# Kernel tuning notes

Measured on AMD Instinct MI355X. Metric: run time of the kernel, lower is better.

The kernel has to match this reference:

```python
import jax, jax.numpy as jnp
import numpy as np
from jax.scipy.special import i0

# --- NUFFT adjoint (Kaiser-Bessel gridding) configuration ---
N = 512            # image side (image_shape)
K = 2 * N
M = 200_000        # n_measurements (visibilities)
B = 8              # batch of measurement vectors
J = 6              # gridding kernel width (plan uses (6, 6))
BETA = 2.34 * J


def setup_inputs() -> dict:
    key = jax.random.key(0)
    k1, k2, k3 = jax.random.split(key, 3)
    # uv coordinates in [-pi, pi) radians per pixel (standard NUFFT convention)
    uv = jax.random.uniform(k1, (M, 2), jnp.float32, -np.pi, np.pi)
    y_real = jax.random.normal(k2, (B, M), jnp.float32)
    y_imag = jax.random.normal(k3, (B, M), jnp.float32)
    weights = jnp.ones((M,), jnp.float32)  # measurement_weights
    return {"y_real": y_real, "y_imag": y_imag, "uv": uv, "weights": weights}


def _grid_1d(coord):
    """Per-axis gridding indices and Kaiser-Bessel weights.

    coord: (M,) frequencies in [-pi, pi). Returns idx (M, J) int32 grid
    columns (wrapped mod K) and w (M, J) float32 kernel weights.
    """
    k = coord / (2.0 * np.pi) * K            # grid units, in [-K/2, K/2)
    km = jnp.floor(k - J / 2.0)              # leftmost neighbor base
    j = jnp.arange(1, J + 1, dtype=k.dtype)
    pts = km[:, None] + j                    # (M, J) grid points covered
    d = k[:, None] - pts                     # signed distance, |d| <= J/2
    arg = jnp.maximum(1.0 - (2.0 * d / J) ** 2, 0.0)
    w = i0(BETA * jnp.sqrt(arg)) / i0(jnp.float32(BETA))
    idx = jnp.mod(pts, K).astype(jnp.int32)
    return idx, w.astype(jnp.float32)


def _deapod(n):
    """Gridding-correction (inverse FT of the KB kernel) at image pixels."""
    x = (jnp.arange(n, dtype=jnp.float32) - n / 2.0) / K
    t = BETA ** 2 - (np.pi * J * x) ** 2
    st = jnp.sqrt(jnp.abs(t))
    num = jnp.where(t > 0, jnp.sinh(st), jnp.sin(st))
    return num / jnp.maximum(st, 1e-6)


def reference(y_real, y_imag, uv, weights):
    y = (y_real + 1j * y_imag).astype(jnp.complex64) * weights  # (B, M)

    ix, wx = _grid_1d(uv[:, 0])  # (M, J)
    iy, wy = _grid_1d(uv[:, 1])  # (M, J)

    # Separable 6x6 kernel: outer products per measurement
    flat_idx = (ix[:, :, None] * K + iy[:, None, :]).reshape(-1)        # (M*J*J,)
    w2 = (wx[:, :, None] * wy[:, None, :]).reshape(M, J * J)            # (M, 36)
    vals = (y[:, :, None] * w2[None]).reshape(B, -1)                    # (B, M*36)

    # Scatter-add onto the oversampled grid (duplicate indices accumulate)
    grid = jnp.zeros((B, K * K), jnp.complex64).at[:, flat_idx].add(vals)
    grid = grid.reshape(B, K, K)

    # Unnormalized inverse FFT (adjoint of the forward FFT), shift to center
    img = jnp.fft.fftshift(jnp.fft.ifft2(grid), axes=(-2, -1)) * (K * K)

    # Crop central N x N region and de-apodize
    s = (K - N) // 2
    img_c = jnp.real(img[:, s:s + N, s:s + N])
    apod = _deapod(N)
    return img_c / (apod[:, None] * apod[None, :])
```

## Files before the change

### kernel.cpp

```cpp
#include <hip/hip_runtime.h>
#include <hip/hip_fp16.h>
#include <math.h>

#define KGRID 1024
#define NIMG  512
#define JW    6
#define BETAF 14.04f
#define NB    8
#define NBIN  16384
#define CAP   96

typedef float v2f __attribute__((ext_vector_type(2)));
typedef float v4f __attribute__((ext_vector_type(4)));

__device__ __forceinline__ float i0f_dev(float x) {
    float ax = fabsf(x);
    if (ax < 3.75f) {
        float z = ax * (1.0f / 3.75f);
        z = z * z;
        return 1.0f + z * (3.5156229f + z * (3.0899424f + z * (1.2067492f +
               z * (0.2659732f + z * (0.0360768f + z * 0.0045813f)))));
    } else {
        float z = 3.75f / ax;
        float p = 0.39894228f + z * (0.01328592f + z * (0.00225319f + z * (-0.00157565f +
                  z * (0.00916281f + z * (-0.02057706f + z * (0.02635537f +
                  z * (-0.01647633f + z * 0.00392377f)))))));
        return expf(ax) * rsqrtf(ax) * p;
    }
}

__global__ __launch_bounds__(256) void prep_kernel(
    const float* __restrict__ yr, const float* __restrict__ yi,
    const float* __restrict__ uv, const float* __restrict__ wts,
    float4* __restrict__ yF4, float4* __restrict__ pnt,
    int* __restrict__ cnt, int* __restrict__ list, int M)
{
    int m = blockIdx.x * 256 + threadIdx.x;
    if (m >= M) return;

    if (m == 0) {
        float4 z = make_float4(0.f, 0.f, 0.f, 0.f);
        #pragma unroll
        for (int q = 0; q < 4; q++) { pnt[(size_t)M * 4 + q] = z; yF4[(size_t)M * 4 + q] = z; }
    }

    float u = uv[2 * m], v = uv[2 * m + 1];
    const float c2g = (float)KGRID / 6.283185307179586f;
    float kx = u * c2g, ky = v * c2g;
    float kmx = floorf(kx - 3.0f), kmy = floorf(ky - 3.0f);
    int x0m = (((int)kmx + 1) + 1024) & 1023;
    int y0m = (((int)kmy + 1) + 1024) & 1023;

    int txA = x0m >> 3, txB = (txA + 1) & 127;
    int tyA = y0m >> 3, tyB = (tyA + 1) & 127;
    bool bx = (x0m & 7) >= 3;
    bool by = (y0m & 7) >= 3;
    int b0 = (txA << 7) | tyA;
    int b1 = (txA << 7) | tyB;
    int b2 = (txB << 7) | tyA;
    int b3 = (txB << 7) | tyB;
    int s0 = atomicAdd(&cnt[b0], 1);
    int s1 = by ? atomicAdd(&cnt[b1], 1) : -1;
    int s2 = bx ? atomicAdd(&cnt[b2], 1) : -1;
    int s3 = (bx && by) ? atomicAdd(&cnt[b3], 1) : -1;

    float inv = 1.0f / i0f_dev(BETAF);
    float s2c = inv * inv;
    float sc = wts[m] * s2c;

    float wx[JW], wy[JW];
    #pragma unroll
    for (int j = 0; j < JW; j++) {
        float dx = kx - kmx - 1.0f - (float)j;
        float rx = dx * (1.0f / 3.0f);
        float ax = fmaxf(1.0f - rx * rx, 0.0f);
        wx[j] = i0f_dev(BETAF * sqrtf(ax)) * sc;
        float dy = ky - kmy - 1.0f - (float)j;
        float ry = dy * (1.0f / 3.0f);
        float ay = fmaxf(1.0f - ry * ry, 0.0f);
        wy[j] = i0f_dev(BETAF * sqrtf(ay));
    }

    float4* p = pnt + (size_t)m * 4;
    p[0] = make_float4(wx[0], wx[1], wx[2], wx[3]);
    p[1] = make_float4(wx[4], wx[5], __int_as_float((x0m << 10) | y0m), 0.0f);
    p[2] = make_float4(wy[0], wy[1], wy[2], wy[3]);
    p[3] = make_float4(wy[4], wy[5], 0.0f, 0.0f);

    #pragma unroll
    for (int bp = 0; bp < 4; bp++) {
        int bb = 2 * bp;
        yF4[(size_t)m * 4 + bp] = make_float4(
            yr[(size_t)bb * M + m],       yi[(size_t)bb * M + m],
            yr[(size_t)(bb + 1) * M + m], yi[(size_t)(bb + 1) * M + m]);
    }

    if ((unsigned)s0 < CAP) list[b0 * CAP + s0] = m;
    if ((unsigned)s1 < CAP) list[b1 * CAP + s1] = m;
    if ((unsigned)s2 < CAP) list[b2 * CAP + s2] = m;
    if ((unsigned)s3 < CAP) list[b3 * CAP + s3] = m;
}

__global__ __launch_bounds__(256) void grid_tile(
    const float* __restrict__ pnt1, const float4* __restrict__ yF4,
    const int* __restrict__ cnt, const int* __restrict__ list,
    __half2* __restrict__ gH, int M)
{
    int lane = threadIdx.x & 63;
    int wid  = threadIdx.x >> 6;
    int tile = blockIdx.x * 4 + wid;
    int tx0 = (tile >> 7) << 3;
    int ty0 = (tile & 127) << 3;
    int lx = lane >> 3, ly = lane & 7;
    int slot = lane & 15;

    v2f acc[NB];
    #pragma unroll
    for (int b = 0; b < NB; b++) acc[b] = (v2f){0.f, 0.f};

    int n = cnt[tile]; if (n > CAP) n = CAP;
    const int* lst = list + tile * CAP;
    const v4f* yV = (const v4f*)yF4;

    int lv0 = (lane < n) ? lst[lane] : M;
    int lv1 = (64 + lane < n && 64 + lane < CAP) ? lst[64 + lane] : M;

    #define FETCH_M(i) __builtin_amdgcn_readlane(((i) < 64) ? lv0 : lv1, (i) & 63)

    int   mA = FETCH_M(0), mB = FETCH_M(1), mC = FETCH_M(2);
    float pwA = pnt1[(size_t)mA * 16 + slot];
    float pwB = pnt1[(size_t)mB * 16 + slot];
    float pwC = pnt1[(size_t)mC * 16 + slot];
    v4f yA0 = yV[(size_t)mA * 4 + 0], yA1 = yV[(size_t)mA * 4 + 1],
        yA2 = yV[(size_t)mA * 4 + 2], yA3 = yV[(size_t)mA * 4 + 3];
    v4f yB0 = yV[(size_t)mB * 4 + 0], yB1 = yV[(size_t)mB * 4 + 1],
        yB2 = yV[(size_t)mB * 4 + 2], yB3 = yV[(size_t)mB * 4 + 3];
    v4f yC0 = yV[(size_t)mC * 4 + 0], yC1 = yV[(size_t)mC * 4 + 1],
        yC2 = yV[(size_t)mC * 4 + 2], yC3 = yV[(size_t)mC * 4 + 3];

    #define PROC(PW, Y0, Y1, Y2, Y3, IDX)                                          \
    {                                                                              \
        int mN = FETCH_M((IDX) + 3);                                               \
        int pwb = __float_as_int(PW);                                              \
        int meta = __builtin_amdgcn_readlane(pwb, 6);                              \
        int j1 = (tx0 + lx - (meta >> 10)) & 1023;                                 \
        int j2 = (ty0 + ly - (meta & 1023)) & 1023;                                \
        int i1 = (j1 < 6) ? j1 : 15;                              \
        int i2 = (j2 < 6) ? (j2 + 8) : 14;                        \
        float wx = __int_as_float(__builtin_amdgcn_ds_bpermute(i1 << 2, pwb));     \
        float wy = __int_as_float(__builtin_amdgcn_ds_bpermute(i2 << 2, pwb));     \
        float w = wx * wy;                                                         \
        v2f w2 = {w, w};                                                           \
        acc[0] = __builtin_elementwise_fma(w2, Y0.xy, acc[0]);                     \
        acc[1] = __builtin_elementwise_fma(w2, Y0.zw, acc[1]);                     \
        acc[2] = __builtin_elementwise_fma(w2, Y1.xy, acc[2]);                     \
        acc[3] = __builtin_elementwise_fma(w2, Y1.zw, acc[3]);                     \
        acc[4] = __builtin_elementwise_fma(w2, Y2.xy, acc[4]);                     \
        acc[5] = __builtin_elementwise_fma(w2, Y2.zw, acc[5]);                     \
        acc[6] = __builtin_elementwise_fma(w2, Y3.xy, acc[6]);                     \
        acc[7] = __builtin_elementwise_fma(w2, Y3.zw, acc[7]);                     \
        PW = pnt1[(size_t)mN * 16 + slot];                                         \
        Y0 = yV[(size_t)mN * 4 + 0];                                               \
        Y1 = yV[(size_t)mN * 4 + 1];                                               \
        Y2 = yV[(size_t)mN * 4 + 2];                                               \
        Y3 = yV[(size_t)mN * 4 + 3];                                               \
    }

    for (int i = 0; i < n; i += 3) {
        PROC(pwA, yA0, yA1, yA2, yA3, i);
        PROC(pwB, yB0, yB1, yB2, yB3, i + 1);
        PROC(pwC, yC0, yC1, yC2, yC3, i + 2);
    }
    #undef PROC
    #undef FETCH_M

    size_t cell = ((size_t)(tx0 + lx) << 10) + (size_t)(ty0 + ly);
    #pragma unroll
    for (int b = 0; b < NB; b++)
        gH[((size_t)b << 20) + cell] = __float22half2_rn(make_float2(acc[b].x, acc[b].y));
}

__device__ __forceinline__ void fft1024_inv(float2* X, float2* Y, const float2* W, int tid)
{
    float2* src = X;
    float2* dst = Y;
    #pragma unroll
    for (int stage = 0; stage < 5; stage++) {
        const int s = 1 << (2 * stage);
        __syncthreads();
        int t = tid;
        int a = t & ~(s - 1);
        float2 x0 = src[t];
        float2 x1 = src[t + 256];
        float2 x2 = src[t + 512];
        float2 x3 = src[t + 768];
        float2 d0 = make_float2(x0.x + x2.x, x0.y + x2.y);
        float2 e0 = make_float2(x0.x - x2.x, x0.y - x2.y);
        float2 d1 = make_float2(x1.x + x3.x, x1.y + x3.y);
        float2 e1 = make_float2(-(x1.y - x3.y), x1.x - x3.x);
        float2 w1 = W[a];
        float2 w2 = W[2 * a];
        float2 w3 = make_float2(w1.x * w2.x - w1.y * w2.y,
                                w1.x * w2.y + w1.y * w2.x);
        int ob = 3 * a + t;
        float2 s0 = make_float2(d0.x + d1.x, d0.y + d1.y);
        float2 s1 = make_float2(e0.x + e1.x, e0.y + e1.y);
        float2 s2 = make_float2(d0.x - d1.x, d0.y - d1.y);
        float2 s3 = make_float2(e0.x - e1.x, e0.y - e1.y);
        dst[ob]         = s0;
        dst[ob + s]     = make_float2(w1.x * s1.x - w1.y * s1.y,
                                      w1.x * s1.y + w1.y * s1.x);
        dst[ob + 2 * s] = make_float2(w2.x * s2.x - w2.y * s2.y,
                                      w2.x * s2.y + w2.y * s2.x);
        dst[ob + 3 * s] = make_float2(w3.x * s3.x - w3.y * s3.y,
                                      w3.x * s3.y + w3.y * s3.x);
        float2* tmp = src; src = dst; dst = tmp;
    }
    __syncthreads();
}

__global__ __launch_bounds__(256) void fft_pass1(const __half2* __restrict__ gH,
                                                 __half2* __restrict__ T)
{
    __shared__ float2 A[1024];
    __shared__ float2 Bb[1024];
    __shared__ float2 W[512];
    __shared__ __half2 R[8][512];

    int blk = blockIdx.x;
    int p   = blk >> 7;
    int g   = blk & 127;
    int tid = threadIdx.x;

    #pragma unroll
    for (int h = 0; h < 2; h++) {
        int j = tid + (h << 8);
        float sn, cn;
        __sincosf(6.283185307179586f * (float)j * (1.0f / 1024.0f), &sn, &cn);
        W[j] = make_float2(cn, sn);
    }

    const __half2* gA = gH + ((size_t)(2 * p)     << 20);
    const __half2* gB = gH + ((size_t)(2 * p + 1) << 20);

    for (int f = 0; f < 8; f++) {
        int k1  = (f < 4) ? (4 * g + f) : (1020 - 4 * g + (f - 4));
        int nk1 = (1024 - k1) & 1023;
        const __half2* rA  = gA + ((size_t)k1  << 10);
        const __half2* rAn = gA + ((size_t)nk1 << 10);
        const __half2* rB  = gB + ((size_t)k1  << 10);
        const __half2* rBn = gB + ((size_t)nk1 << 10);
        __syncthreads();
        #pragma unroll
        for (int h = 0; h < 4; h++) {
            int k2  = tid + (h << 8);
            int nk2 = (1024 - k2) & 1023;
            float2 va  = __half22float2(rA[k2]);
            float2 van = __half22float2(rAn[nk2]);
            float2 vb  = __half22float2(rB[k2]);
            float2 vbn = __half22float2(rBn[nk2]);
            A[k2] = make_float2(0.5f * (va.x + van.x) - 0.5f * (vb.y - vbn.y),
                                0.5f * (va.y - van.y) + 0.5f * (vb.x + vbn.x));
        }
        fft1024_inv(A, Bb, W, tid);
        #pragma unroll
        for (int h = 0; h < 2; h++) {
            int xo2 = tid + (h << 8);
            R[f][xo2] = __float22half2_rn(Bb[(xo2 + 768) & 1023]);
        }
    }
    __syncthreads();

    #pragma unroll
    for (int h = 0; h < 2; h++) {
        int xo2 = tid + (h << 8);
        __half2* Trow = T + (((size_t)p * 512 + xo2) << 10);
        int4 q0, q1;
        q0.x = *(const int*)&R[0][xo2]; q0.y = *(const int*)&R[1][xo2];
        q0.z = *(const int*)&R[2][xo2]; q0.w = *(const int*)&R[3][xo2];
        q1.x = *(const int*)&R[4][xo2]; q1.y = *(const int*)&R[5][xo2];
        q1.z = *(const int*)&R[6][xo2]; q1.w = *(const int*)&R[7][xo2];
        *(int4*)(Trow + 4 * g)          = q0;
        *(int4*)(Trow + (1020 - 4 * g)) = q1;
    }
}

__device__ __forceinline__ float apodf(int n) {
    float x  = ((float)n - 256.0f) * (1.0f / 1024.0f);
    float px = 3.14159265358979f * 6.0f * x;
    float t  = BETAF * BETAF - px * px;
    float st = sqrtf(fabsf(t));
    float num = (t > 0.0f) ? sinhf(st) : __sinf(st);
    return num / fmaxf(st, 1e-6f);
}

__global__ __launch_bounds__(256) void fft_pass2(const __half2* __restrict__ T,
                                                 float* __restrict__ out)
{
    __shared__ float2 A[1024];
    __shared__ float2 Bb[1024];
    __shared__ float2 W[512];
    __shared__ float2 R[4][512];

    int blk = blockIdx.x;
    int p   = blk >> 7;
    int xg  = blk & 127;
    int tid = threadIdx.x;

    #pragma unroll
    for (int h = 0; h < 2; h++) {
        int j = tid + (h << 8);
        float sn, cn;
        __sincosf(6.283185307179586f * (float)j * (1.0f / 1024.0f), &sn, &cn);
        W[j] = make_float2(cn, sn);
    }

    float a2[4];
    #pragma unroll
    for (int r = 0; r < 4; r++) a2[r] = apodf((xg << 2) + r);

    for (int r = 0; r < 4; r++) {
        int xo2 = (xg << 2) + r;
        const __half2* row = T + (((size_t)p * 512 + xo2) << 10);
        __syncthreads();
        #pragma unroll
        for (int h = 0; h < 4; h++) {
            int i = tid + (h << 8);
            A[i] = __half22float2(row[i]);
        }
        fft1024_inv(A, Bb, W, tid);
        #pragma unroll
        for (int h = 0; h < 2; h++) {
            int xo1 = tid + (h << 8);
            float2 v = Bb[(xo1 + 768) & 1023];
            R[r][xo1] = make_float2(v.x / a2[r], v.y / a2[r]);
        }
    }
    __syncthreads();

    int b0 = 2 * p;
    #pragma unroll
    for (int h = 0; h < 2; h++) {
        int xo1 = tid + (h << 8);
        float inva1 = 1.0f / apodf(xo1);
        float2 f0 = R[0][xo1], f1 = R[1][xo1], f2 = R[2][xo1], f3 = R[3][xo1];
        float4* o0 = (float4*)(out + (((size_t)b0 * 512 + xo1) << 9) + (xg << 2));
        float4* o1 = (float4*)(out + (((size_t)(b0 + 1) * 512 + xo1) << 9) + (xg << 2));
        *o0 = make_float4(f0.x * inva1, f1.x * inva1, f2.x * inva1, f3.x * inva1);
        *o1 = make_float4(f0.y * inva1, f1.y * inva1, f2.y * inva1, f3.y * inva1);
    }
}

extern "C" void kernel_launch(void* const* d_in, const int* in_sizes, int n_in,
                              void* d_out, int out_size, void* d_ws, size_t ws_size,
                              hipStream_t stream)
{
    const float* yr  = (const float*)d_in[0];
    const float* yi  = (const float*)d_in[1];
    const float* uv  = (const float*)d_in[2];
    const float* wts = (const float*)d_in[3];

    int M = in_sizes[3];

    __half2* gH = (__half2*)d_ws;
    __half2* T  = (__half2*)((char*)d_ws + ((size_t)32 << 20));
    char*    p2 = (char*)d_ws + ((size_t)64 << 20);
    int*    cnt  = (int*)p2;
    int*    list = (int*)(p2 + 65536);
    float4* yF4  = (float4*)(p2 + 6553600);
    float4* pnt  = (float4*)(p2 + 19500032);

    hipMemsetAsync(cnt, 0, NBIN * sizeof(int), stream);
    prep_kernel<<<dim3((M + 255) / 256), dim3(256), 0, stream>>>(
        yr, yi, uv, wts, yF4, pnt, cnt, list, M);
    grid_tile<<<dim3(NBIN / 4), dim3(256), 0, stream>>>(
        (const float*)pnt, (const float4*)yF4, cnt, list, gH, M);
    fft_pass1<<<dim3(4 * 128), dim3(256), 0, stream>>>(gH, T);
    fft_pass2<<<dim3(4 * 128), dim3(256), 0, stream>>>(T, (float*)d_out);
}
```

Measured before the change: 172.0 us.

## Software-pipeline gridding weights one step ahead and double FFT block counts

The gridding loop now unrolls by four measurements and computes the bpermute-based kernel weight for the next measurement before issuing the FMAs for the current one, so the LDS permute latency can overlap with accumulation. Both FFT passes halve the rows handled per block and double the grid to 1024 blocks, trading per-block twiddle setup and narrower stores for more parallelism and occupancy on the GPU. The extra prefetch register set raises register pressure in the gridding kernel.

```diff
diff --git a/kernel.cpp b/kernel.cpp
--- a/kernel.cpp
+++ b/kernel.cpp
@@ -127,30 +127,41 @@
 
     #define FETCH_M(i) __builtin_amdgcn_readlane(((i) < 64) ? lv0 : lv1, (i) & 63)
 
-    int   mA = FETCH_M(0), mB = FETCH_M(1), mC = FETCH_M(2);
+    int   mA = FETCH_M(0), mB = FETCH_M(1), mC = FETCH_M(2), mD = FETCH_M(3);
     float pwA = pnt1[(size_t)mA * 16 + slot];
     float pwB = pnt1[(size_t)mB * 16 + slot];
     float pwC = pnt1[(size_t)mC * 16 + slot];
+    float pwD = pnt1[(size_t)mD * 16 + slot];
     v4f yA0 = yV[(size_t)mA * 4 + 0], yA1 = yV[(size_t)mA * 4 + 1],
         yA2 = yV[(size_t)mA * 4 + 2], yA3 = yV[(size_t)mA * 4 + 3];
     v4f yB0 = yV[(size_t)mB * 4 + 0], yB1 = yV[(size_t)mB * 4 + 1],
         yB2 = yV[(size_t)mB * 4 + 2], yB3 = yV[(size_t)mB * 4 + 3];
     v4f yC0 = yV[(size_t)mC * 4 + 0], yC1 = yV[(size_t)mC * 4 + 1],
         yC2 = yV[(size_t)mC * 4 + 2], yC3 = yV[(size_t)mC * 4 + 3];
-
-    #define PROC(PW, Y0, Y1, Y2, Y3, IDX)                                          \
+    v4f yD0 = yV[(size_t)mD * 4 + 0], yD1 = yV[(size_t)mD * 4 + 1],
+        yD2 = yV[(size_t)mD * 4 + 2], yD3 = yV[(size_t)mD * 4 + 3];
+
+    #define COMPW(PW, WOUT)                                                        \
     {                                                                              \
-        int mN = FETCH_M((IDX) + 3);                                               \
         int pwb = __float_as_int(PW);                                              \
         int meta = __builtin_amdgcn_readlane(pwb, 6);                              \
         int j1 = (tx0 + lx - (meta >> 10)) & 1023;                                 \
         int j2 = (ty0 + ly - (meta & 1023)) & 1023;                                \
         int i1 = (j1 < 6) ? j1 : 15;                              \
         int i2 = (j2 < 6) ? (j2 + 8) : 14;                        \
-        float wx = __int_as_float(__builtin_amdgcn_ds_bpermute(i1 << 2, pwb));     \
-        float wy = __int_as_float(__builtin_amdgcn_ds_bpermute(i2 << 2, pwb));     \
-        float w = wx * wy;                                                         \
-        v2f w2 = {w, w};                                                           \
+        float wxv = __int_as_float(__builtin_amdgcn_ds_bpermute(i1 << 2, pwb));    \
+        float wyv = __int_as_float(__builtin_amdgcn_ds_bpermute(i2 << 2, pwb));    \
+        WOUT = wxv * wyv;                                                          \
+    }
+
+    float wCur;
+    COMPW(pwA, wCur);
+
+    #define PROC(PW_NEXT, PW_SELF, Y0, Y1, Y2, Y3, IDX)                            \
+    {                                                                              \
+        int mN = FETCH_M((IDX) + 4);                                               \
+        float wNext; COMPW(PW_NEXT, wNext);                                        \
+        v2f w2 = {wCur, wCur};                                                     \
         acc[0] = __builtin_elementwise_fma(w2, Y0.xy, acc[0]);                     \
         acc[1] = __builtin_elementwise_fma(w2, Y0.zw, acc[1]);                     \
         acc[2] = __builtin_elementwise_fma(w2, Y1.xy, acc[2]);                     \
@@ -159,19 +170,22 @@
         acc[5] = __builtin_elementwise_fma(w2, Y2.zw, acc[5]);                     \
         acc[6] = __builtin_elementwise_fma(w2, Y3.xy, acc[6]);                     \
         acc[7] = __builtin_elementwise_fma(w2, Y3.zw, acc[7]);                     \
-        PW = pnt1[(size_t)mN * 16 + slot];                                         \
+        wCur = wNext;                                                              \
+        PW_SELF = pnt1[(size_t)mN * 16 + slot];                                    \
         Y0 = yV[(size_t)mN * 4 + 0];                                               \
         Y1 = yV[(size_t)mN * 4 + 1];                                               \
         Y2 = yV[(size_t)mN * 4 + 2];                                               \
         Y3 = yV[(size_t)mN * 4 + 3];                                               \
     }
 
-    for (int i = 0; i < n; i += 3) {
-        PROC(pwA, yA0, yA1, yA2, yA3, i);
-        PROC(pwB, yB0, yB1, yB2, yB3, i + 1);
-        PROC(pwC, yC0, yC1, yC2, yC3, i + 2);
+    for (int i = 0; i < n; i += 4) {
+        PROC(pwB, pwA, yA0, yA1, yA2, yA3, i);
+        PROC(pwC, pwB, yB0, yB1, yB2, yB3, i + 1);
+        PROC(pwD, pwC, yC0, yC1, yC2, yC3, i + 2);
+        PROC(pwA, pwD, yD0, yD1, yD2, yD3, i + 3);
     }
     #undef PROC
+    #undef COMPW
     #undef FETCH_M
 
     size_t cell = ((size_t)(tx0 + lx) << 10) + (size_t)(ty0 + ly);
@@ -225,11 +239,11 @@
     __shared__ float2 A[1024];
     __shared__ float2 Bb[1024];
     __shared__ float2 W[512];
-    __shared__ __half2 R[8][512];
+    __shared__ __half2 R[4][512];
 
     int blk = blockIdx.x;
-    int p   = blk >> 7;
-    int g   = blk & 127;
+    int p   = blk >> 8;
+    int g   = blk & 255;
     int tid = threadIdx.x;
 
     #pragma unroll
@@ -243,8 +257,8 @@
     const __half2* gA = gH + ((size_t)(2 * p)     << 20);
     const __half2* gB = gH + ((size_t)(2 * p + 1) << 20);
 
-    for (int f = 0; f < 8; f++) {
-        int k1  = (f < 4) ? (4 * g + f) : (1020 - 4 * g + (f - 4));
+    for (int f = 0; f < 4; f++) {
+        int k1  = (f < 2) ? (2 * g + f) : (1022 - 2 * g + (f - 2));
         int nk1 = (1024 - k1) & 1023;
         const __half2* rA  = gA + ((size_t)k1  << 10);
         const __half2* rAn = gA + ((size_t)nk1 << 10);
@@ -275,13 +289,11 @@
     for (int h = 0; h < 2; h++) {
         int xo2 = tid + (h << 8);
         __half2* Trow = T + (((size_t)p * 512 + xo2) << 10);
-        int4 q0, q1;
+        int2 q0, q1;
         q0.x = *(const int*)&R[0][xo2]; q0.y = *(const int*)&R[1][xo2];
-        q0.z = *(const int*)&R[2][xo2]; q0.w = *(const int*)&R[3][xo2];
-        q1.x = *(const int*)&R[4][xo2]; q1.y = *(const int*)&R[5][xo2];
-        q1.z = *(const int*)&R[6][xo2]; q1.w = *(const int*)&R[7][xo2];
-        *(int4*)(Trow + 4 * g)          = q0;
-        *(int4*)(Trow + (1020 - 4 * g)) = q1;
+        q1.x = *(const int*)&R[2][xo2]; q1.y = *(const int*)&R[3][xo2];
+        *(int2*)(Trow + 2 * g)          = q0;
+        *(int2*)(Trow + (1022 - 2 * g)) = q1;
     }
 }
 
@@ -300,11 +312,11 @@
     __shared__ float2 A[1024];
     __shared__ float2 Bb[1024];
     __shared__ float2 W[512];
-    __shared__ float2 R[4][512];
+    __shared__ float2 R[2][512];
 
     int blk = blockIdx.x;
-    int p   = blk >> 7;
-    int xg  = blk & 127;
+    int p   = blk >> 8;
+    int xg  = blk & 255;
     int tid = threadIdx.x;
 
     #pragma unroll
@@ -315,12 +327,12 @@
         W[j] = make_float2(cn, sn);
     }
 
-    float a2[4];
-    #pragma unroll
-    for (int r = 0; r < 4; r++) a2[r] = apodf((xg << 2) + r);
-
-    for (int r = 0; r < 4; r++) {
-        int xo2 = (xg << 2) + r;
+    float a2[2];
+    #pragma unroll
+    for (int r = 0; r < 2; r++) a2[r] = apodf((xg << 1) + r);
+
+    for (int r = 0; r < 2; r++) {
+        int xo2 = (xg << 1) + r;
         const __half2* row = T + (((size_t)p * 512 + xo2) << 10);
         __syncthreads();
         #pragma unroll
@@ -343,11 +355,11 @@
     for (int h = 0; h < 2; h++) {
         int xo1 = tid + (h << 8);
         float inva1 = 1.0f / apodf(xo1);
-        float2 f0 = R[0][xo1], f1 = R[1][xo1], f2 = R[2][xo1], f3 = R[3][xo1];
-        float4* o0 = (float4*)(out + (((size_t)b0 * 512 + xo1) << 9) + (xg << 2));
-        float4* o1 = (float4*)(out + (((size_t)(b0 + 1) * 512 + xo1) << 9) + (xg << 2));
-        *o0 = make_float4(f0.x * inva1, f1.x * inva1, f2.x * inva1, f3.x * inva1);
-        *o1 = make_float4(f0.y * inva1, f1.y * inva1, f2.y * inva1, f3.y * inva1);
+        float2 f0 = R[0][xo1], f1 = R[1][xo1];
+        float2* o0 = (float2*)(out + (((size_t)b0 * 512 + xo1) << 9) + (xg << 1));
+        float2* o1 = (float2*)(out + (((size_t)(b0 + 1) * 512 + xo1) << 9) + (xg << 1));
+        *o0 = make_float2(f0.x * inva1, f1.x * inva1);
+        *o1 = make_float2(f0.y * inva1, f1.y * inva1);
     }
 }
 
@@ -375,6 +387,6 @@
         yr, yi, uv, wts, yF4, pnt, cnt, list, M);
     grid_tile<<<dim3(NBIN / 4), dim3(256), 0, stream>>>(
         (const float*)pnt, (const float4*)yF4, cnt, list, gH, M);
-    fft_pass1<<<dim3(4 * 128), dim3(256), 0, stream>>>(gH, T);
-    fft_pass2<<<dim3(4 * 128), dim3(256), 0, stream>>>(T, (float*)d_out);
-}
+    fft_pass1<<<dim3(4 * 256), dim3(256), 0, stream>>>(gH, T);
+    fft_pass2<<<dim3(4 * 256), dim3(256), 0, stream>>>(T, (float*)d_out);
+}
```

Measured after the change: 178.2 us. 3.6% more time.
